# Kernel tuning notes

Hardware: AMD Instinct MI355X
Metric: run time of the kernel (lower is better)

Reference implementation:

```python
import jax, jax.numpy as jnp
import numpy as np

B, T, V = 128, 4096, 32
NGRAN, NGLIMPSE, NHID = 2, 32, 256
GWIDTH = 0.25
BIG = 1e10  # pad key for masked-out timesteps


def setup_inputs() -> dict:
    key = jax.random.key(0)
    ks = jax.random.split(key, 6)
    vals = jax.random.normal(ks[0], (B, T, V), jnp.float32)
    # irregular but time-ordered observation times in [0, 100)
    time = jnp.sort(jax.random.uniform(ks[1], (B, T), jnp.float32) * 100.0, axis=1)
    masks = jax.random.randint(ks[2], (B, T, V), 0, 2).astype(jnp.int32)
    lengths = jnp.sum(masks[:, :, 0], axis=1).astype(jnp.int32)
    l_t = jax.random.uniform(ks[3], (B, 1), jnp.float32)
    fan_in = V * NGRAN * NGLIMPSE + 1
    W = jax.random.normal(ks[4], (NHID, fan_in), jnp.float32) / np.sqrt(fan_in)
    b = jnp.zeros((NHID,), jnp.float32)
    return {"vals": vals, "time": time, "masks": masks, "lengths": lengths,
            "l_t": l_t, "W": W, "b": b}


def _glimpse_offsets():
    # getGlimpseTimesteps: two scales i in (1, 5); shape [nglimpse, ngran]
    return jnp.stack([jnp.linspace(-GWIDTH * i / 2.0, GWIDTH * i / 2.0, NGLIMPSE)
                      for i in (1, 5)], axis=1)


def _glimpses(vals, time, masks, l_t):
    # Vectorized ragged masked linear interpolation over all (b, v) pairs.
    m = masks > 0                                          # [B,T,V]
    key = jnp.where(m, time[:, :, None], BIG)              # masked-out -> BIG
    order = jnp.argsort(key, axis=1)                       # valid (sorted) first
    ts = jnp.take_along_axis(key, order, axis=1)           # [B,T,V]
    vs = jnp.take_along_axis(vals, order, axis=1)          # [B,T,V]
    nv = jnp.sum(m, axis=1)                                # [B,V] num valid
    tmax = jnp.max(jnp.where(m, time[:, :, None], -jnp.inf), axis=1)
    tmax = jnp.where(nv > 0, tmax, 0.0)                    # [B,V]

    offs = _glimpse_offsets()                              # [nglimpse, ngran]
    # q[b,v,g,k] = (offs[k,g] + l_t[b]) * tmax[b,v]  (denormalize by per-var max t)
    loc = offs.T[None, None] + l_t[:, 0][:, None, None, None]   # [B,1,ngran,nglimpse]
    q = loc * tmax[:, :, None, None]                       # [B,V,ngran,nglimpse]
    Q = NGRAN * NGLIMPSE
    qf = q.reshape(q.shape[0], q.shape[1], Q)              # [B,V,Q] (G-major order)

    ts_bv = jnp.moveaxis(ts, 1, 2)                         # [B,V,T]
    vs_bv = jnp.moveaxis(vs, 1, 2)                         # [B,V,T]
    idx = jax.vmap(jax.vmap(jnp.searchsorted))(ts_bv, qf)  # [B,V,Q]
    hi = jnp.maximum(nv - 1, 0)[:, :, None]
    left = jnp.clip(idx - 1, 0, hi)
    right = jnp.clip(idx, 0, hi)
    t_l = jnp.take_along_axis(ts_bv, left, axis=-1)
    t_r = jnp.take_along_axis(ts_bv, right, axis=-1)
    v_l = jnp.take_along_axis(vs_bv, left, axis=-1)
    v_r = jnp.take_along_axis(vs_bv, right, axis=-1)
    denom = t_r - t_l
    safe = jnp.where(denom > 0, denom, 1.0)
    w = jnp.where(denom > 0, (qf - t_l) / safe, 0.0)
    # out-of-range queries clamp to endpoint values (scipy fill_value=(v[0], v[-1]))
    out = v_l + w * (v_r - v_l)
    # num_vals==1 -> constant value (falls out of clamping); num_vals==0 -> zeros
    out = jnp.where(nv[:, :, None] > 0, out, 0.0)
    return out.reshape(out.shape[0], -1)                   # [B, V*ngran*nglimpse]


def reference(vals, time, masks, lengths, l_t, W, b):
    g = _glimpses(vals, time, masks, l_t)                  # [B, V*ngran*nglimpse]
    grep = jnp.concatenate([g, l_t], axis=1) @ W.T + b     # [B, nhid]
    return grep, g[:, g.shape[1] // 2]
```

## Files before the change

### kernel.cpp

```cpp
#include <hip/hip_runtime.h>

typedef unsigned long long ull;

#define B_    128
#define T_    4096
#define V_    32
#define NHID  256
#define GDIM  2048
#define GW    0.25f
#define CAP   3584

__global__ __launch_bounds__(512, 4) void glimpse_kernel(
    const float* __restrict__ vals, const float* __restrict__ time_,
    const int* __restrict__ masks, const float* __restrict__ l_t,
    float* __restrict__ g_ws, float* __restrict__ mid_out)
{
    __shared__ float time_s[T_];
    __shared__ unsigned short idx_c[8][CAP];
    __shared__ unsigned char  cnt8[16][8][8];
    __shared__ unsigned short pref[16][8];
    __shared__ unsigned short wavepre[16][8][8];
    __shared__ int nv_s[8];

    int bid = blockIdx.x;
    int wg  = (bid & 7) * 64 + (bid >> 3);
    int b   = wg >> 2;
    int v0  = (wg & 3) * 8;

    int tid = threadIdx.x, lane = tid & 63, wave = tid >> 6;
    int vq = tid & 1, tl = tid >> 1;

    {
        const float4* trow4 = (const float4*)(time_ + (long)b * T_);
        float4* ts4 = (float4*)time_s;
        for (int i = tid; i < T_ / 4; i += 512) ts4[i] = trow4[i];
    }

    const int* mbase = masks + ((long)b * T_) * V_ + v0 + vq * 4;
    ull qm  = vq ? 0xAAAAAAAAAAAAAAAAull : 0x5555555555555555ull;
    ull ltm = (1ull << lane) - 1ull;

    unsigned f0 = 0, f1 = 0, f2 = 0, f3 = 0;

    #pragma unroll 4
    for (int c = 0; c < 16; ++c) {
        int t = c * 256 + tl;
        int4 m4 = *reinterpret_cast<const int4*>(mbase + (long)t * V_);
        ull bl0 = __ballot(m4.x != 0);
        ull bl1 = __ballot(m4.y != 0);
        ull bl2 = __ballot(m4.z != 0);
        ull bl3 = __ballot(m4.w != 0);
        f0 |= (unsigned)(m4.x != 0) << c;
        f1 |= (unsigned)(m4.y != 0) << c;
        f2 |= (unsigned)(m4.z != 0) << c;
        f3 |= (unsigned)(m4.w != 0) << c;
        if (lane < 8) {
            int li = lane & 3;
            ull bs = (li == 0) ? bl0 : (li == 1) ? bl1 : (li == 2) ? bl2 : bl3;
            ull qq = (lane >> 2) ? 0xAAAAAAAAAAAAAAAAull : 0x5555555555555555ull;
            cnt8[c][wave][lane] = (unsigned char)__popcll(bs & qq);
        }
    }
    __syncthreads();

    if (tid < 128) {
        int c = tid >> 3, v = tid & 7;
        int s = 0;
        #pragma unroll
        for (int w = 0; w < 8; ++w) s += cnt8[c][w][v];
        pref[c][v] = (unsigned short)s;
    }
    __syncthreads();
    if (tid < 8) {
        int run = 0;
        for (int c = 0; c < 16; ++c) {
            int x = pref[c][tid];
            pref[c][tid] = (unsigned short)run;
            run += x;
        }
        nv_s[tid] = (run < CAP) ? run : CAP;
    }
    __syncthreads();
    if (tid < 128) {
        int c = tid >> 3, v = tid & 7;
        int run = pref[c][v];
        #pragma unroll
        for (int w = 0; w < 8; ++w) {
            wavepre[c][w][v] = (unsigned short)run;
            run += cnt8[c][w][v];
        }
    }
    __syncthreads();

    int vb = vq * 4;
    #pragma unroll 4
    for (int c = 0; c < 16; ++c) {
        unsigned short t = (unsigned short)(c * 256 + tl);
        ull bl0 = __ballot((f0 >> c) & 1);
        ull bl1 = __ballot((f1 >> c) & 1);
        ull bl2 = __ballot((f2 >> c) & 1);
        ull bl3 = __ballot((f3 >> c) & 1);
        if ((f0 >> c) & 1) { int r = wavepre[c][wave][vb+0] + (int)__popcll(bl0 & qm & ltm); if (r < CAP) idx_c[vb+0][r] = t; }
        if ((f1 >> c) & 1) { int r = wavepre[c][wave][vb+1] + (int)__popcll(bl1 & qm & ltm); if (r < CAP) idx_c[vb+1][r] = t; }
        if ((f2 >> c) & 1) { int r = wavepre[c][wave][vb+2] + (int)__popcll(bl2 & qm & ltm); if (r < CAP) idx_c[vb+2][r] = t; }
        if ((f3 >> c) & 1) { int r = wavepre[c][wave][vb+3] + (int)__popcll(bl3 & qm & ltm); if (r < CAP) idx_c[vb+3][r] = t; }
    }
    __syncthreads();

    int v  = wave;
    int j  = lane;
    int gs = j >> 5, k = j & 31;
    int nv = nv_s[v];
    float ltv = l_t[b];
    int vg = v0 + v;

    float outv = 0.0f;
    if (nv > 0) {
        float tmax = time_s[idx_c[v][nv - 1]];
        float hw  = GW * (gs ? 5.0f : 1.0f) * 0.5f;
        float off = -hw + (float)k * (2.0f * hw / 31.0f);
        float qv  = (off + ltv) * tmax;
        int lo = 0, hi = nv;
        while (lo < hi) {
            int mid = (lo + hi) >> 1;
            float tm = time_s[idx_c[v][mid]];
            if (tm < qv) lo = mid + 1; else hi = mid;
        }
        int left  = lo - 1; if (left < 0) left = 0; if (left > nv - 1) left = nv - 1;
        int right = lo;     if (right > nv - 1) right = nv - 1;
        int til = idx_c[v][left], tir = idx_c[v][right];
        float tle = time_s[til], tre = time_s[tir];
        float vle = vals[((long)b * T_ + til) * V_ + vg];
        float vre = vals[((long)b * T_ + tir) * V_ + vg];
        float den = tre - tle;
        float wt  = (den > 0.0f) ? (qv - tle) / den : 0.0f;
        outv = vle + wt * (vre - vle);
    }
    int col = vg * 64 + j;
    g_ws[(long)b * GDIM + col] = outv;
    if (col == 1024) mid_out[b] = outv;
}

__global__ __launch_bounds__(256) void grep_kernel(
    const float* __restrict__ g_ws, const float* __restrict__ l_t,
    const float* __restrict__ W, const float* __restrict__ bias,
    float* __restrict__ out)
{
    int bid = blockIdx.x;
    int w2 = (bid & 7) * 32 + (bid >> 3);
    int ht = w2 >> 3;
    int bg = w2 & 7;
    int tid = threadIdx.x, lane = tid & 63, wave = tid >> 6;
    int b0 = bg * 16 + wave * 4;
    int h0 = ht * 8;

    float ga[4][32];
    #pragma unroll
    for (int i = 0; i < 4; ++i) {
        #pragma unroll
        for (int c = 0; c < 32; ++c)
            ga[i][c] = g_ws[(long)(b0 + i) * GDIM + c * 64 + lane];
    }
    float lt0 = l_t[b0], lt1 = l_t[b0+1], lt2 = l_t[b0+2], lt3 = l_t[b0+3];

    for (int hh = 0; hh < 8; ++hh) {
        int h = h0 + hh;
        const float* wr = W + (long)h * (GDIM + 1);
        float a0 = 0.f, a1 = 0.f, a2 = 0.f, a3 = 0.f;
        #pragma unroll
        for (int c = 0; c < 32; ++c) {
            float wv = wr[c * 64 + lane];
            a0 += wv * ga[0][c];
            a1 += wv * ga[1][c];
            a2 += wv * ga[2][c];
            a3 += wv * ga[3][c];
        }
        if (lane == 0) {
            float wl = wr[GDIM];
            a0 += wl * lt0; a1 += wl * lt1; a2 += wl * lt2; a3 += wl * lt3;
        }
        #pragma unroll
        for (int s = 32; s; s >>= 1) {
            a0 += __shfl_xor(a0, s, 64);
            a1 += __shfl_xor(a1, s, 64);
            a2 += __shfl_xor(a2, s, 64);
            a3 += __shfl_xor(a3, s, 64);
        }
        if (lane == 0) {
            float bv = bias[h];
            out[(long)(b0 + 0) * NHID + h] = a0 + bv;
            out[(long)(b0 + 1) * NHID + h] = a1 + bv;
            out[(long)(b0 + 2) * NHID + h] = a2 + bv;
            out[(long)(b0 + 3) * NHID + h] = a3 + bv;
        }
    }
}

extern "C" void kernel_launch(void* const* d_in, const int* in_sizes, int n_in,
                              void* d_out, int out_size, void* d_ws, size_t ws_size,
                              hipStream_t stream)
{
    const float* vals  = (const float*)d_in[0];
    const float* time_ = (const float*)d_in[1];
    const int*   masks = (const int*)d_in[2];
    const float* l_t   = (const float*)d_in[4];
    const float* W     = (const float*)d_in[5];
    const float* bias  = (const float*)d_in[6];

    float* out  = (float*)d_out;
    float* g_ws = (float*)d_ws;

    glimpse_kernel<<<B_ * 4, 512, 0, stream>>>(vals, time_, masks, l_t,
                                               g_ws, out + (long)B_ * NHID);
    grep_kernel<<<256, 256, 0, stream>>>(g_ws, l_t, W, bias, out);
}
```

Before: 175.5 us.

## Replace compaction with mask bitmaps and rank-select interpolation lookup

```diff
diff --git a/kernel.cpp b/kernel.cpp
--- a/kernel.cpp
+++ b/kernel.cpp
@@ -8,135 +8,158 @@
 #define NHID  256
 #define GDIM  2048
 #define GW    0.25f
-#define CAP   3584
-
-__global__ __launch_bounds__(512, 4) void glimpse_kernel(
-    const float* __restrict__ vals, const float* __restrict__ time_,
-    const int* __restrict__ masks, const float* __restrict__ l_t,
-    float* __restrict__ g_ws, float* __restrict__ mid_out)
-{
-    __shared__ float time_s[T_];
-    __shared__ unsigned short idx_c[8][CAP];
-    __shared__ unsigned char  cnt8[16][8][8];
-    __shared__ unsigned short pref[16][8];
-    __shared__ unsigned short wavepre[16][8][8];
-    __shared__ int nv_s[8];
-
+
+__global__ __launch_bounds__(256) void mask_kernel(
+    const int* __restrict__ masks, ull* __restrict__ gm)
+{
     int bid = blockIdx.x;
-    int wg  = (bid & 7) * 64 + (bid >> 3);
-    int b   = wg >> 2;
-    int v0  = (wg & 3) * 8;
+    int wg  = (bid & 7) * 256 + (bid >> 3);
+    int vq4 = wg & 3;
+    int tq  = (wg >> 2) & 3;
+    int b   = wg >> 4;
 
     int tid = threadIdx.x, lane = tid & 63, wave = tid >> 6;
     int vq = tid & 1, tl = tid >> 1;
 
+    const int* mbase = masks + ((long)b * T_) * V_ + vq4 * 8 + vq * 4;
+    int wbase = (b * 4 + vq4) * 4 * 128 + tq * 32 + wave;
+
+    int4 m[8];
+    #pragma unroll
+    for (int c = 0; c < 8; ++c)
+        m[c] = *reinterpret_cast<const int4*>(mbase + (long)(tq*1024 + c*128 + tl) * V_);
+
+    #pragma unroll
+    for (int c = 0; c < 8; ++c) {
+        ull bl0 = __ballot(m[c].x != 0);
+        ull bl1 = __ballot(m[c].y != 0);
+        ull bl2 = __ballot(m[c].z != 0);
+        ull bl3 = __ballot(m[c].w != 0);
+        if (lane < 4) {
+            ull w = (lane == 0) ? bl0 : (lane == 1) ? bl1 : (lane == 2) ? bl2 : bl3;
+            gm[wbase + lane * 128 + c * 4] = w;
+        }
+    }
+}
+
+__global__ __launch_bounds__(256) void query_kernel(
+    const float* __restrict__ vals, const float* __restrict__ time_,
+    const ull* __restrict__ gm, const float* __restrict__ l_t,
+    float* __restrict__ g_ws, float* __restrict__ mid_out)
+{
+    __shared__ float time_s[T_];
+    __shared__ ull   mask64[4][128];
+    __shared__ unsigned short rank16[4][128];
+    __shared__ int   nv_s[4];
+    __shared__ float tmax_s[4];
+
+    int bid = blockIdx.x;
+    int wg  = (bid & 7) * 128 + (bid >> 3);
+    int b   = wg >> 3;
+    int vg  = wg & 7;
+    int vq4 = vg >> 1, par = vg & 1;
+
+    int tid = threadIdx.x, lane = tid & 63, wave = tid >> 6;
+
     {
-        const float4* trow4 = (const float4*)(time_ + (long)b * T_);
-        float4* ts4 = (float4*)time_s;
-        for (int i = tid; i < T_ / 4; i += 512) ts4[i] = trow4[i];
-    }
-
-    const int* mbase = masks + ((long)b * T_) * V_ + v0 + vq * 4;
-    ull qm  = vq ? 0xAAAAAAAAAAAAAAAAull : 0x5555555555555555ull;
-    ull ltm = (1ull << lane) - 1ull;
-
-    unsigned f0 = 0, f1 = 0, f2 = 0, f3 = 0;
-
-    #pragma unroll 4
-    for (int c = 0; c < 16; ++c) {
-        int t = c * 256 + tl;
-        int4 m4 = *reinterpret_cast<const int4*>(mbase + (long)t * V_);
-        ull bl0 = __ballot(m4.x != 0);
-        ull bl1 = __ballot(m4.y != 0);
-        ull bl2 = __ballot(m4.z != 0);
-        ull bl3 = __ballot(m4.w != 0);
-        f0 |= (unsigned)(m4.x != 0) << c;
-        f1 |= (unsigned)(m4.y != 0) << c;
-        f2 |= (unsigned)(m4.z != 0) << c;
-        f3 |= (unsigned)(m4.w != 0) << c;
-        if (lane < 8) {
-            int li = lane & 3;
-            ull bs = (li == 0) ? bl0 : (li == 1) ? bl1 : (li == 2) ? bl2 : bl3;
-            ull qq = (lane >> 2) ? 0xAAAAAAAAAAAAAAAAull : 0x5555555555555555ull;
-            cnt8[c][wave][lane] = (unsigned char)__popcll(bs & qq);
-        }
+        const float4* t4 = (const float4*)(time_ + (long)b * T_);
+        float4* s4 = (float4*)time_s;
+        #pragma unroll
+        for (int i = 0; i < 4; ++i) s4[tid + i * 256] = t4[tid + i * 256];
+        const ull* src = gm + (long)(b * 4 + vq4) * 4 * 128;
+        ((ull*)mask64)[tid]       = src[tid];
+        ((ull*)mask64)[tid + 256] = src[tid + 256];
     }
     __syncthreads();
 
-    if (tid < 128) {
-        int c = tid >> 3, v = tid & 7;
-        int s = 0;
-        #pragma unroll
-        for (int w = 0; w < 8; ++w) s += cnt8[c][w][v];
-        pref[c][v] = (unsigned short)s;
+    ull pm = 0x5555555555555555ull << par;
+
+    {
+        ull w0 = mask64[wave][2*lane]     & pm;
+        ull w1 = mask64[wave][2*lane + 1] & pm;
+        int pa = __popcll(w0), pb = __popcll(w1);
+        int x = pa + pb, inc = x;
+        #pragma unroll
+        for (int off = 1; off < 64; off <<= 1) {
+            int y = __shfl_up(inc, off, 64);
+            if (lane >= off) inc += y;
+        }
+        int excl = inc - x;
+        rank16[wave][2*lane]     = (unsigned short)excl;
+        rank16[wave][2*lane + 1] = (unsigned short)(excl + pa);
+        if (lane == 63) nv_s[wave] = inc;
+        ull nzball = __ballot((w0 | w1) != 0ull);
+        if (nzball) {
+            int hl = 63 - __clzll(nzball);
+            if (lane == hl) {
+                ull wsel = w1 ? w1 : w0;
+                int widx = 2*lane + (w1 ? 1 : 0);
+                int bp = 63 - __clzll(wsel);
+                tmax_s[wave] = time_s[widx * 32 + (bp >> 1)];
+            }
+        }
     }
     __syncthreads();
-    if (tid < 8) {
-        int run = 0;
-        for (int c = 0; c < 16; ++c) {
-            int x = pref[c][tid];
-            pref[c][tid] = (unsigned short)run;
-            run += x;
-        }
-        nv_s[tid] = (run < CAP) ? run : CAP;
-    }
-    __syncthreads();
-    if (tid < 128) {
-        int c = tid >> 3, v = tid & 7;
-        int run = pref[c][v];
-        #pragma unroll
-        for (int w = 0; w < 8; ++w) {
-            wavepre[c][w][v] = (unsigned short)run;
-            run += cnt8[c][w][v];
-        }
-    }
-    __syncthreads();
-
-    int vb = vq * 4;
-    #pragma unroll 4
-    for (int c = 0; c < 16; ++c) {
-        unsigned short t = (unsigned short)(c * 256 + tl);
-        ull bl0 = __ballot((f0 >> c) & 1);
-        ull bl1 = __ballot((f1 >> c) & 1);
-        ull bl2 = __ballot((f2 >> c) & 1);
-        ull bl3 = __ballot((f3 >> c) & 1);
-        if ((f0 >> c) & 1) { int r = wavepre[c][wave][vb+0] + (int)__popcll(bl0 & qm & ltm); if (r < CAP) idx_c[vb+0][r] = t; }
-        if ((f1 >> c) & 1) { int r = wavepre[c][wave][vb+1] + (int)__popcll(bl1 & qm & ltm); if (r < CAP) idx_c[vb+1][r] = t; }
-        if ((f2 >> c) & 1) { int r = wavepre[c][wave][vb+2] + (int)__popcll(bl2 & qm & ltm); if (r < CAP) idx_c[vb+2][r] = t; }
-        if ((f3 >> c) & 1) { int r = wavepre[c][wave][vb+3] + (int)__popcll(bl3 & qm & ltm); if (r < CAP) idx_c[vb+3][r] = t; }
-    }
-    __syncthreads();
-
-    int v  = wave;
-    int j  = lane;
-    int gs = j >> 5, k = j & 31;
-    int nv = nv_s[v];
-    float ltv = l_t[b];
-    int vg = v0 + v;
-
+
+    int v   = wave;
+    int vgl = vq4 * 8 + par * 4 + v;
+    int j   = lane, gs = j >> 5, k = j & 31;
+    int nv  = nv_s[v];
     float outv = 0.0f;
     if (nv > 0) {
-        float tmax = time_s[idx_c[v][nv - 1]];
         float hw  = GW * (gs ? 5.0f : 1.0f) * 0.5f;
         float off = -hw + (float)k * (2.0f * hw / 31.0f);
-        float qv  = (off + ltv) * tmax;
-        int lo = 0, hi = nv;
-        while (lo < hi) {
-            int mid = (lo + hi) >> 1;
-            float tm = time_s[idx_c[v][mid]];
-            if (tm < qv) lo = mid + 1; else hi = mid;
-        }
-        int left  = lo - 1; if (left < 0) left = 0; if (left > nv - 1) left = nv - 1;
-        int right = lo;     if (right > nv - 1) right = nv - 1;
-        int til = idx_c[v][left], tir = idx_c[v][right];
-        float tle = time_s[til], tre = time_s[tir];
-        float vle = vals[((long)b * T_ + til) * V_ + vg];
-        float vre = vals[((long)b * T_ + tir) * V_ + vg];
+        float qv  = (off + l_t[b]) * tmax_s[v];
+
+        int lo = 0, hi = T_;
+        while (lo < hi) { int mid = (lo + hi) >> 1;
+                          if (time_s[mid] < qv) lo = mid + 1; else hi = mid; }
+        int p = lo;
+
+        int r;
+        if (p >= T_) r = nv;
+        else {
+            int wr = p >> 5, tin = p & 31;
+            ull below = tin ? ((1ull << (2 * tin)) - 1ull) : 0ull;
+            r = (int)rank16[v][wr] + __popcll(mask64[v][wr] & pm & below);
+        }
+        int rc = (r > nv - 1) ? nv - 1 : r;
+        int lc = r - 1; if (lc < 0) lc = 0; if (lc > nv - 1) lc = nv - 1;
+
+        int ws = 0;
+        #pragma unroll
+        for (int s = 64; s; s >>= 1) {
+            int t2 = ws + s;
+            if (t2 < 128 && (int)rank16[v][t2] <= rc) ws = t2;
+        }
+        int jj = rc - (int)rank16[v][ws];
+        ull ww = mask64[v][ws] & pm;
+        int bitpos = 0;
+        #pragma unroll
+        for (int half = 32; half; half >>= 1) {
+            ull lm = (half == 32) ? 0xFFFFFFFFull : ((1ull << half) - 1ull);
+            int c = __popcll(ww & lm);
+            if (jj >= c) { jj -= c; ww >>= half; bitpos += half; }
+        }
+        int sel_r = ws * 32 + (bitpos >> 1);
+
+        int sel_l = sel_r;
+        if (lc != rc) {
+            ull wb = mask64[v][ws] & pm & (bitpos ? ((1ull << bitpos) - 1ull) : 0ull);
+            int wsx = ws;
+            while (!wb) { --wsx; wb = mask64[v][wsx] & pm; }
+            int bp = 63 - __clzll(wb);
+            sel_l = wsx * 32 + (bp >> 1);
+        }
+
+        float tle = time_s[sel_l], tre = time_s[sel_r];
+        float vle = vals[((long)b * T_ + sel_l) * V_ + vgl];
+        float vre = vals[((long)b * T_ + sel_r) * V_ + vgl];
         float den = tre - tle;
         float wt  = (den > 0.0f) ? (qv - tle) / den : 0.0f;
         outv = vle + wt * (vre - vle);
     }
-    int col = vg * 64 + j;
+    int col = vgl * 64 + j;
     g_ws[(long)b * GDIM + col] = outv;
     if (col == 1024) mid_out[b] = outv;
 }
@@ -147,51 +170,43 @@
     float* __restrict__ out)
 {
     int bid = blockIdx.x;
-    int w2 = (bid & 7) * 32 + (bid >> 3);
-    int ht = w2 >> 3;
-    int bg = w2 & 7;
+    int wg = (bid & 7) * 128 + (bid >> 3);
+    int hg = wg >> 4;
+    int bg = wg & 15;
     int tid = threadIdx.x, lane = tid & 63, wave = tid >> 6;
-    int b0 = bg * 16 + wave * 4;
-    int h0 = ht * 8;
-
-    float ga[4][32];
-    #pragma unroll
-    for (int i = 0; i < 4; ++i) {
-        #pragma unroll
-        for (int c = 0; c < 32; ++c)
-            ga[i][c] = g_ws[(long)(b0 + i) * GDIM + c * 64 + lane];
-    }
-    float lt0 = l_t[b0], lt1 = l_t[b0+1], lt2 = l_t[b0+2], lt3 = l_t[b0+3];
-
-    for (int hh = 0; hh < 8; ++hh) {
+    int b0 = bg * 8 + wave * 2;
+    int h0 = hg * 4;
+
+    float4 ga[2][8];
+    #pragma unroll
+    for (int i = 0; i < 2; ++i)
+        #pragma unroll
+        for (int c = 0; c < 8; ++c)
+            ga[i][c] = *(const float4*)(g_ws + (long)(b0 + i) * GDIM + c * 256 + lane * 4);
+    float lt0 = l_t[b0], lt1 = l_t[b0 + 1];
+
+    #pragma unroll
+    for (int hh = 0; hh < 4; ++hh) {
         int h = h0 + hh;
         const float* wr = W + (long)h * (GDIM + 1);
-        float a0 = 0.f, a1 = 0.f, a2 = 0.f, a3 = 0.f;
-        #pragma unroll
-        for (int c = 0; c < 32; ++c) {
-            float wv = wr[c * 64 + lane];
-            a0 += wv * ga[0][c];
-            a1 += wv * ga[1][c];
-            a2 += wv * ga[2][c];
-            a3 += wv * ga[3][c];
-        }
-        if (lane == 0) {
-            float wl = wr[GDIM];
-            a0 += wl * lt0; a1 += wl * lt1; a2 += wl * lt2; a3 += wl * lt3;
-        }
+        float a0 = 0.f, a1 = 0.f;
+        #pragma unroll
+        for (int c = 0; c < 8; ++c) {
+            const float* wp = wr + c * 256 + lane * 4;
+            float w0 = wp[0], w1 = wp[1], w2 = wp[2], w3 = wp[3];
+            a0 += w0*ga[0][c].x + w1*ga[0][c].y + w2*ga[0][c].z + w3*ga[0][c].w;
+            a1 += w0*ga[1][c].x + w1*ga[1][c].y + w2*ga[1][c].z + w3*ga[1][c].w;
+        }
+        if (lane == 0) { float wl = wr[GDIM]; a0 += wl * lt0; a1 += wl * lt1; }
         #pragma unroll
         for (int s = 32; s; s >>= 1) {
             a0 += __shfl_xor(a0, s, 64);
             a1 += __shfl_xor(a1, s, 64);
-            a2 += __shfl_xor(a2, s, 64);
-            a3 += __shfl_xor(a3, s, 64);
         }
         if (lane == 0) {
             float bv = bias[h];
             out[(long)(b0 + 0) * NHID + h] = a0 + bv;
             out[(long)(b0 + 1) * NHID + h] = a1 + bv;
-            out[(long)(b0 + 2) * NHID + h] = a2 + bv;
-            out[(long)(b0 + 3) * NHID + h] = a3 + bv;
         }
     }
 }
@@ -209,8 +224,10 @@
 
     float* out  = (float*)d_out;
     float* g_ws = (float*)d_ws;
-
-    glimpse_kernel<<<B_ * 4, 512, 0, stream>>>(vals, time_, masks, l_t,
-                                               g_ws, out + (long)B_ * NHID);
-    grep_kernel<<<256, 256, 0, stream>>>(g_ws, l_t, W, bias, out);
-}
+    ull*   gm   = (ull*)((char*)d_ws + (1 << 20));
+
+    mask_kernel <<<2048, 256, 0, stream>>>(masks, gm);
+    query_kernel<<<1024, 256, 0, stream>>>(vals, time_, gm, l_t,
+                                           g_ws, out + (long)B_ * NHID);
+    grep_kernel <<<1024, 256, 0, stream>>>(g_ws, l_t, W, bias, out);
+}
```

Result: faster. 165.0 us (-6.0%).
